# Kernel tuning notes

Measured on AMD Instinct MI355X. Metric: run time of the kernel, lower is better.

The kernel has to match this reference:

```python
import jax, jax.numpy as jnp
import numpy as np
import math

MID = 48       # mid_channels
HEADS = 4      # num_heads
POS = 16       # mid_channels // 3 (row/col positional channels)


def _unfold(x, p):
    """nn.Unfold with kernel p, padding p//2: (..., H, W) -> (..., p, p, H, W)."""
    H, W = x.shape[-2], x.shape[-1]
    pad = p // 2
    xp = jnp.pad(x, [(0, 0)] * (x.ndim - 2) + [(pad, pad), (pad, pad)])
    return jnp.stack(
        [jnp.stack([xp[..., k:k + H, l:l + W] for l in range(p)], axis=-3)
         for k in range(p)], axis=-4)


def _pe_mlp(idx, w1, b1, g, b, w2, b2):
    """Conv2d(1->16,1x1) -> LayerNorm(16) -> Swish -> Conv2d(16->POS,1x1) on scalar coords."""
    t = idx.reshape(-1, 1)                         # (N,1)
    h = t @ w1.T + b1                              # (N,16)
    mu = jnp.mean(h, -1, keepdims=True)
    var = jnp.var(h, -1, keepdims=True)
    h = (h - mu) * jax.lax.rsqrt(var + 1e-5) * g + b
    h = h * jax.nn.sigmoid(h)                      # Swish
    e = h @ w2.T + b2                              # (N,POS)
    return e.reshape(idx.shape + (e.shape[-1],))   # (V,P,P,POS)


def setup_inputs() -> dict:
    key = jax.random.key(0)
    ks = jax.random.split(key, 32)
    B, Cin, G, H, W, P, Cout = 2, 32, 4, 28, 28, 7, 64

    def n(k, shp, s=0.05):
        return jax.random.normal(k, shp, dtype=jnp.float32) * s

    inp = {"x": jax.random.normal(ks[0], (B, Cin, G, H, W), dtype=jnp.float32)}
    inp["Wq"] = n(ks[1], (MID * HEADS, Cin)); inp["bq"] = n(ks[2], (MID * HEADS,))
    inp["Wk"] = n(ks[3], (MID * HEADS, Cin)); inp["bk"] = n(ks[4], (MID * HEADS,))
    inp["Wv"] = n(ks[5], (MID * HEADS, Cin)); inp["bv"] = n(ks[6], (MID * HEADS,))
    inp["Wout"] = n(ks[7], (Cout, MID * HEADS)); inp["bout"] = n(ks[8], (Cout,))
    inp["row_w1"] = n(ks[9], (16, 1)); inp["row_b1"] = n(ks[10], (16,))
    inp["row_ln_g"] = jnp.ones((16,), jnp.float32); inp["row_ln_b"] = jnp.zeros((16,), jnp.float32)
    inp["row_w2"] = n(ks[11], (POS, 16)); inp["row_b2"] = n(ks[12], (POS,))
    inp["col_w1"] = n(ks[13], (16, 1)); inp["col_b1"] = n(ks[14], (16,))
    inp["col_ln_g"] = jnp.ones((16,), jnp.float32); inp["col_ln_b"] = jnp.zeros((16,), jnp.float32)
    inp["col_w2"] = n(ks[15], (POS, 16)); inp["col_b2"] = n(ks[16], (POS,))
    inp["group_emb"] = n(ks[17], (G, MID - 2 * POS))
    # rotated relative spatial positions, normalized to [-1, 1]
    lin = np.linspace(-1.0, 1.0, P).astype(np.float32)
    r = np.repeat(lin[:, None], P, 1)
    c = np.repeat(lin[None, :], P, 0)
    rows, cols = [], []
    for v in range(G):
        th = v * math.pi / 2.0
        rows.append(math.cos(th) * r - math.sin(th) * c)
        cols.append(math.sin(th) * r + math.cos(th) * c)
    inp["row_indices"] = jnp.asarray(np.stack(rows, 0))
    inp["col_indices"] = jnp.asarray(np.stack(cols, 0))
    # acted relative group positions for cyclic group C4
    ar = np.arange(G)
    gi = (ar[:, None, None] + ar[None, None, :] - ar[None, :, None]) % G
    inp["g_indices"] = jnp.asarray(gi, dtype=jnp.int32)
    return inp


def _forward(x, Wq, bq, Wk, bk, Wv, bv, Wout, bout,
             row_w1, row_b1, row_ln_g, row_ln_b, row_w2, row_b2,
             col_w1, col_b1, col_ln_g, col_ln_b, col_w2, col_b2,
             group_emb, row_indices, col_indices, g_indices):
    B, Cin, G, H, W = x.shape
    P = row_indices.shape[-1]
    sqn = jnp.sqrt(jnp.float32(Cin))

    def proj(Wm, bm):  # 1x1 Conv3d -> (B, MID, HEADS, G, H, W)
        y = jnp.einsum('oi,bigyx->bogyx', Wm, x) + bm[None, :, None, None, None]
        return y.reshape(B, MID, HEADS, G, H, W)

    q = proj(Wq, bq)
    k = proj(Wk, bk)
    v = proj(Wv, bv)
    k_loc = _unfold(k, P)   # (B, MID, HEADS, G, P, P, H, W)
    v_loc = _unfold(v, P)

    content = jnp.einsum('bchgij,bchmklij->bhgijmkl', q, k_loc)
    row_e = _pe_mlp(row_indices, row_w1, row_b1, row_ln_g, row_ln_b, row_w2, row_b2)
    col_e = _pe_mlp(col_indices, col_w1, col_b1, col_ln_g, col_ln_b, col_w2, col_b2)
    row_s = jnp.einsum('bchgij,vklc->bhvgijkl', q[:, :POS], row_e)
    col_s = jnp.einsum('bchgij,vklc->bhvgijkl', q[:, POS:2 * POS], col_e)
    g_e = group_emb[g_indices]                              # (V, G, M, gdim)
    g_s = jnp.einsum('bchgij,vgmc->bhvgijm', q[:, 2 * POS:], g_e)

    # scores: (b, h, v, g, i, j, m, k, l)
    scores = (row_s[:, :, :, :, :, :, None] + col_s[:, :, :, :, :, :, None]
              + g_s[..., None, None] + content[:, :, None]) / sqn

    # mask patch positions that fall outside the image (-inf -> prob 0)
    valid = _unfold(jnp.ones((H, W), jnp.float32), P)       # (P, P, H, W)
    valid = jnp.transpose(valid, (2, 3, 0, 1))[None, None, None, None, :, :, None, :, :]
    scores = jnp.where(valid > 0.5, scores, -jnp.inf)

    shp = scores.shape
    probs = jax.nn.softmax(scores.reshape(shp[:-3] + (-1,)), axis=-1).reshape(shp)

    o = jnp.einsum('bhvgijmkl,bchmklij->bchvij', probs, v_loc)  # (B, MID, HEADS, V, H, W)
    o = o.reshape(B, MID * HEADS, G, H, W)
    return jnp.einsum('oi,bivyx->bovyx', Wout, o) + bout[None, :, None, None, None]


def reference(x, Wq, bq, Wk, bk, Wv, bv, Wout, bout,
              row_w1, row_b1, row_ln_g, row_ln_b, row_w2, row_b2,
              col_w1, col_b1, col_ln_g, col_ln_b, col_w2, col_b2,
              group_emb, row_indices, col_indices, g_indices):
    return _forward(x, Wq, bq, Wk, bk, Wv, bv, Wout, bout,
                    row_w1, row_b1, row_ln_g, row_ln_b, row_w2, row_b2,
                    col_w1, col_b1, col_ln_g, col_ln_b, col_w2, col_b2,
                    group_emb, row_indices, col_indices, g_indices)
```

## Files before the change

### kernel.cpp

```cpp
#include <hip/hip_runtime.h>
#include <math.h>

#define Bb   2
#define CIN  32
#define Gg   4
#define NH   4
#define Hh   28
#define Ww   28
#define HW   784
#define Pp   7
#define PP   49
#define MID  48
#define COUT 64
#define OC   192

#define QF    0
#define KF    602112
#define VF    1204224
#define OOFF  1806336
#define KBH   75264
#define KM    18816
#define VBH   75264
#define VPL   37632

#define KSCALE 0.2550611135387359f

__device__ unsigned g_peT2[Gg * PP * 16];
__device__ unsigned g_geT2[8 * 64];
__device__ float    g_WT2[OC * COUT];

typedef _Float16 h2f __attribute__((ext_vector_type(2)));

__device__ __forceinline__ unsigned packh2(float a, float b) {
    auto r = __builtin_amdgcn_cvt_pkrtz(a, b);
    return __builtin_bit_cast(unsigned, r);
}

__device__ __forceinline__ float fdot2(unsigned a, unsigned b, float c) {
    return __builtin_amdgcn_fdot2(__builtin_bit_cast(h2f, a),
                                  __builtin_bit_cast(h2f, b), c, false);
}

__device__ __forceinline__ float exp2_fast(float x) {
    float r;
    asm("v_exp_f32 %0, %1" : "=v"(r) : "v"(x));
    return r;
}

__device__ __forceinline__ void conv7x2(const float4* __restrict__ Wr4, float bias,
                                        const float* __restrict__ x0,
                                        const float* __restrict__ x1,
                                        float* a0, float* a1) {
    float4 w[8];
    #pragma unroll
    for (int t = 0; t < 8; t++) w[t] = Wr4[t];
    #pragma unroll
    for (int jj = 0; jj < 7; jj++) { a0[jj] = bias; a1[jj] = bias; }
    #pragma unroll
    for (int ci8 = 0; ci8 < 8; ci8++) {
        int cb = ci8 * 4;
#define CH1(WV, CI, XR, A)                                                    \
        {   float wv = WV;                                                    \
            float4 xA = *(const float4*)&XR[(CI) * 8];                        \
            float4 xB = *(const float4*)&XR[(CI) * 8 + 4];                    \
            A[0] += wv * xA.x; A[1] += wv * xA.y; A[2] += wv * xA.z;          \
            A[3] += wv * xA.w; A[4] += wv * xB.x; A[5] += wv * xB.y;          \
            A[6] += wv * xB.z; }
        CH1(w[ci8].x, cb + 0, x0, a0) CH1(w[ci8].x, cb + 0, x1, a1)
        CH1(w[ci8].y, cb + 1, x0, a0) CH1(w[ci8].y, cb + 1, x1, a1)
        CH1(w[ci8].z, cb + 2, x0, a0) CH1(w[ci8].z, cb + 2, x1, a1)
        CH1(w[ci8].w, cb + 3, x0, a0) CH1(w[ci8].w, cb + 3, x1, a1)
#undef CH1
    }
}

__global__ __launch_bounds__(192) void qkvpe_kernel(const float* __restrict__ x,
    const float* __restrict__ Wq, const float* __restrict__ bq,
    const float* __restrict__ Wk, const float* __restrict__ bk,
    const float* __restrict__ Wv, const float* __restrict__ bv,
    const float* row_w1, const float* row_b1,
    const float* row_g,  const float* row_bb,
    const float* row_w2, const float* row_b2,
    const float* col_w1, const float* col_b1,
    const float* col_g,  const float* col_bb,
    const float* col_w2, const float* col_b2,
    const float* row_idx, const float* col_idx,
    const float* group_emb, const int* g_indices,
    const float* Wout,
    float* __restrict__ ws)
{
    __shared__ float xs[2 * CIN * 8];
    __shared__ float wtmp[16 * 193];
    int tid = threadIdx.x;
    unsigned* uw = (unsigned*)ws;
    if (blockIdx.x == Bb * 2 * Hh * 4) {
        for (int t = tid; t < 2 * Gg * PP; t += 192) {
            int half = t / (Gg * PP);
            int n    = t - half * (Gg * PP);
            int v = n / PP, kl = n % PP;
            const float* w1 = half ? col_w1 : row_w1;
            const float* b1 = half ? col_b1 : row_b1;
            const float* lg = half ? col_g  : row_g;
            const float* lb = half ? col_bb : row_bb;
            const float* w2 = half ? col_w2 : row_w2;
            const float* b2 = half ? col_b2 : row_b2;
            float tv = half ? col_idx[n] : row_idx[n];

            float hb[16];
            float mean = 0.f;
            for (int k = 0; k < 16; k++) { hb[k] = tv * w1[k] + b1[k]; mean += hb[k]; }
            mean *= (1.f / 16.f);
            float var = 0.f;
            for (int k = 0; k < 16; k++) { float d = hb[k] - mean; var += d * d; }
            var *= (1.f / 16.f);
            float inv = 1.f / sqrtf(var + 1e-5f);
            for (int k = 0; k < 16; k++) {
                float hn = (hb[k] - mean) * inv * lg[k] + lb[k];
                hb[k] = hn / (1.f + expf(-hn));
            }
            float accv[16];
            for (int p = 0; p < 16; p++) {
                float acc = b2[p];
                for (int k = 0; k < 16; k++) acc += hb[k] * w2[p * 16 + k];
                accv[p] = acc * KSCALE;
            }
            for (int i2 = 0; i2 < 8; i2++)
                g_peT2[(v * PP + kl) * 16 + half * 8 + i2] =
                    packh2(accv[2 * i2], accv[2 * i2 + 1]);
        }
        for (int t = tid; t < 64; t += 192) {
            int gi = g_indices[t];
            for (int i2 = 0; i2 < 8; i2++)
                g_geT2[i2 * 64 + t] = packh2(group_emb[gi * 16 + 2 * i2] * KSCALE,
                                             group_emb[gi * 16 + 2 * i2 + 1] * KSCALE);
        }
        for (int chunk = 0; chunk < 4; chunk++) {
            int obase = chunk * 16;
            __syncthreads();
            for (int idx = tid; idx < 16 * OC; idx += 192) {
                int ol = idx / OC, t = idx % OC;
                wtmp[ol * 193 + t] = Wout[(obase + ol) * OC + t];
            }
            __syncthreads();
            for (int idx = tid; idx < 16 * OC; idx += 192) {
                int tp = idx / 16, ol = idx % 16;
                int h = tp / MID, c = tp % MID;
                g_WT2[tp * 64 + obase + ol] = wtmp[ol * 193 + c * NH + h];
            }
        }
        return;
    }

    int r = blockIdx.x;
    int jq = r & 3; r >>= 2;
    int i = r % Hh; r /= Hh;
    int gp = r & 1; int b = r >> 1;
    int j0 = jq * 7;

    for (int idx = tid; idx < 2 * CIN * 7; idx += 192) {
        int gs = idx / (CIN * 7), rem = idx % (CIN * 7);
        int ci = rem / 7, jj = rem % 7;
        xs[gs * CIN * 8 + ci * 8 + jj] =
            x[((b * CIN + ci) * Gg + 2 * gp + gs) * HW + i * Ww + j0 + jj];
    }
    __syncthreads();

    int h = tid / MID, c = tid % MID;
    int oo = c * NH + h;
    int bh = b * NH + h;
    int ij0 = i * Ww + j0;
    const float* xs0 = &xs[0];
    const float* xs1 = &xs[CIN * 8];

    float a0[7], a1[7];
    conv7x2((const float4*)(Wq + oo * CIN), bq[oo], xs0, xs1, a0, a1);
    {
        int ob0 = QF + ((bh * Gg + 2 * gp + 0) * HW + ij0) * 24 + (c >> 1);
        int ob1 = QF + ((bh * Gg + 2 * gp + 1) * HW + ij0) * 24 + (c >> 1);
        #pragma unroll
        for (int jj = 0; jj < 7; jj++) {
            float p0 = __shfl_xor(a0[jj], 1, 64);
            float p1 = __shfl_xor(a1[jj], 1, 64);
            if (!(tid & 1)) {
                uw[ob0 + jj * 24] = packh2(a0[jj], p0);
                uw[ob1 + jj * 24] = packh2(a1[jj], p1);
            }
        }
    }
    conv7x2((const float4*)(Wk + oo * CIN), bk[oo], xs0, xs1, a0, a1);
    {
        int ob0 = KF + ((bh * Gg + 2 * gp + 0) * HW + ij0) * 24 + (c >> 1);
        int ob1 = KF + ((bh * Gg + 2 * gp + 1) * HW + ij0) * 24 + (c >> 1);
        #pragma unroll
        for (int jj = 0; jj < 7; jj++) {
            float v0 = a0[jj] * KSCALE, v1 = a1[jj] * KSCALE;
            float p0 = __shfl_xor(v0, 1, 64);
            float p1 = __shfl_xor(v1, 1, 64);
            if (!(tid & 1)) {
                uw[ob0 + jj * 24] = packh2(v0, p0);
                uw[ob1 + jj * 24] = packh2(v1, p1);
            }
        }
    }
    conv7x2((const float4*)(Wv + oo * CIN), bv[oo], xs0, xs1, a0, a1);
    {
        int vb = VF + ((bh * 2 + gp) * HW + ij0) * 48 + c;
        #pragma unroll
        for (int jj = 0; jj < 7; jj++)
            uw[vb + jj * 48] = packh2(a0[jj], a1[jj]);
    }
}

__global__ __launch_bounds__(256, 4) void attn_kernel(float* __restrict__ ws)
{
    __shared__ __align__(16) unsigned kvb[7000];
    __shared__ __align__(16) unsigned pp2[4][PP][8];
    __shared__ __align__(16) unsigned qp[4][4][32];
    __shared__ __align__(16) float gsm[4][64];

    const int tid  = threadIdx.x;
    const int wave = tid >> 6;
    const int lane = tid & 63;

    int blk = blockIdx.x;
    int j0 = (blk % 7) * 4;
    int i  = (blk / 7) % Hh;
    int bh = blk / (7 * Hh);
    int b = bh >> 2, h = bh & 3;
    int j  = j0 + wave;
    int ij = i * Ww + j;

    const unsigned* uw = (const unsigned*)ws;
    const unsigned* Kf = uw + KF + bh * KBH;
    const unsigned* Vf = uw + VF + bh * VBH;
    float* Ot = ws + OOFF;

    if (lane < 48) {
        int g = lane / 12, c4 = lane % 12;
        uint2 qv = *(const uint2*)&uw[QF + ((bh * Gg + g) * HW + ij) * 24 + c4 * 2];
        qp[wave][g][c4 * 2]     = qv.x;
        qp[wave][g][c4 * 2 + 1] = qv.y;
    }

    #pragma unroll
    for (int s = 0; s < 2; s++) {
        int t = tid + s * 256;
        if (t < 420) {
            int c8 = t % 6, cl = t / 6;
            int gy = i - 3 + cl / 10, gx = j0 - 3 + cl % 10;
            gy = min(max(gy, 0), Hh - 1); gx = min(max(gx, 0), Ww - 1);
            const unsigned* kp = &Kf[(gy * Ww + gx) * 24 + c8 * 4];
            #pragma unroll
            for (int m = 0; m < 4; m++) {
                uint4 kv = *(const uint4*)(kp + m * KM);
                int o = (m * 70 + cl) * 25 + c8 * 4;
                *(uint2*)&kvb[o]     = make_uint2(kv.x, kv.y);
                *(uint2*)&kvb[o + 2] = make_uint2(kv.z, kv.w);
            }
        }
    }

    int kk = lane / Pp, ll = lane % Pp;
    int cell = (lane < PP) ? kk * 10 + ll + wave : 0;
    bool vmask = (lane < PP) && ((unsigned)(i + kk - 3) < Hh) && ((unsigned)(j + ll - 3) < Ww);
    int lclamp = lane < PP ? lane : 0;

    float per[4][4] = {};
    #pragma unroll
    for (int u4 = 0; u4 < 4; u4++) {
        uint4 qA = *(const uint4*)&qp[wave][0][u4 * 4];
        uint4 qB = *(const uint4*)&qp[wave][1][u4 * 4];
        uint4 qC = *(const uint4*)&qp[wave][2][u4 * 4];
        uint4 qD = *(const uint4*)&qp[wave][3][u4 * 4];
        #pragma unroll
        for (int v = 0; v < 4; v++) {
            uint4 pk = *(const uint4*)&g_peT2[(v * PP + lclamp) * 16 + u4 * 4];
            per[v][0] = fdot2(pk.w, qA.w, fdot2(pk.z, qA.z, fdot2(pk.y, qA.y, fdot2(pk.x, qA.x, per[v][0]))));
            per[v][1] = fdot2(pk.w, qB.w, fdot2(pk.z, qB.z, fdot2(pk.y, qB.y, fdot2(pk.x, qB.x, per[v][1]))));
            per[v][2] = fdot2(pk.w, qC.w, fdot2(pk.z, qC.z, fdot2(pk.y, qC.y, fdot2(pk.x, qC.x, per[v][2]))));
            per[v][3] = fdot2(pk.w, qD.w, fdot2(pk.z, qD.z, fdot2(pk.y, qD.y, fdot2(pk.x, qD.x, per[v][3]))));
        }
    }
    if (!vmask) {
        #pragma unroll
        for (int v = 0; v < 4; v++)
            #pragma unroll
            for (int g = 0; g < 4; g++) per[v][g] = -INFINITY;
    }

    {
        int g = (lane >> 2) & 3;
        float ga = 0.f;
        #pragma unroll
        for (int u = 0; u < 8; u++)
            ga = fdot2(g_geT2[u * 64 + lane], qp[wave][g][16 + u], ga);
        gsm[wave][lane] = ga;
    }
    __syncthreads();

    float acc[4][4] = {};
    #pragma unroll 2
    for (int u4 = 0; u4 < 6; u4++) {
        uint4 qA = *(const uint4*)&qp[wave][0][u4 * 4];
        uint4 qB = *(const uint4*)&qp[wave][1][u4 * 4];
        uint4 qC = *(const uint4*)&qp[wave][2][u4 * 4];
        uint4 qD = *(const uint4*)&qp[wave][3][u4 * 4];
        #pragma unroll
        for (int m = 0; m < 4; m++) {
            int base = (m * 70 + cell) * 25 + u4 * 4;
            uint2 k01 = *(const uint2*)&kvb[base];
            uint2 k23 = *(const uint2*)&kvb[base + 2];
            acc[m][0] = fdot2(k23.y, qA.w, fdot2(k23.x, qA.z, fdot2(k01.y, qA.y, fdot2(k01.x, qA.x, acc[m][0]))));
            acc[m][1] = fdot2(k23.y, qB.w, fdot2(k23.x, qB.z, fdot2(k01.y, qB.y, fdot2(k01.x, qB.x, acc[m][1]))));
            acc[m][2] = fdot2(k23.y, qC.w, fdot2(k23.x, qC.z, fdot2(k01.y, qC.y, fdot2(k01.x, qC.x, acc[m][2]))));
            acc[m][3] = fdot2(k23.y, qD.w, fdot2(k23.x, qD.z, fdot2(k01.y, qD.y, fdot2(k01.x, qD.x, acc[m][3]))));
        }
    }

    float ppr[4][4] = {};
    #pragma unroll
    for (int v = 0; v < 4; v++) {
        #pragma unroll
        for (int g = 0; g < 4; g++) {
            int vg = v * 4 + g;
            float4 gs = *(const float4*)&gsm[wave][vg * 4];
            float ex[4];
            ex[0] = exp2_fast(acc[0][g] + per[v][g] + gs.x);
            ex[1] = exp2_fast(acc[1][g] + per[v][g] + gs.y);
            ex[2] = exp2_fast(acc[2][g] + per[v][g] + gs.z);
            ex[3] = exp2_fast(acc[3][g] + per[v][g] + gs.w);
            float ls = ex[0] + ex[1] + ex[2] + ex[3];
            #pragma unroll
            for (int d = 32; d > 0; d >>= 1) ls += __shfl_xor(ls, d, 64);
            float rinv = 1.0f / ls;
            #pragma unroll
            for (int m = 0; m < 4; m++) ppr[v][m] += ex[m] * rinv;
        }
    }
    if (lane < PP) {
        uint4 w0, w1;
        w0.x = packh2(ppr[0][0], ppr[0][1]); w0.y = packh2(ppr[0][2], ppr[0][3]);
        w0.z = packh2(ppr[1][0], ppr[1][1]); w0.w = packh2(ppr[1][2], ppr[1][3]);
        w1.x = packh2(ppr[2][0], ppr[2][1]); w1.y = packh2(ppr[2][2], ppr[2][3]);
        w1.z = packh2(ppr[3][0], ppr[3][1]); w1.w = packh2(ppr[3][2], ppr[3][3]);
        *(uint4*)&pp2[wave][lane][0] = w0;
        *(uint4*)&pp2[wave][lane][4] = w1;
    }
    __syncthreads();

    for (int t = tid; t < 840; t += 256) {
        int c4 = t % 12, cl = t / 12;
        int gy = i - 3 + cl / 10, gx = j0 - 3 + cl % 10;
        gy = min(max(gy, 0), Hh - 1); gx = min(max(gx, 0), Ww - 1);
        int off = (gy * Ww + gx) * 48 + c4 * 4;
        uint4 A = *(const uint4*)&Vf[off];
        uint4 B = *(const uint4*)&Vf[VPL + off];
        int o = cl * 48 + c4 * 4;
        *(uint4*)&kvb[o]        = A;
        *(uint4*)&kvb[3360 + o] = B;
    }
    __syncthreads();

    if (lane < MID) {
        float o0 = 0.f, o1 = 0.f, o2 = 0.f, o3 = 0.f;
        const uint4* ppw = (const uint4*)&pp2[wave][0][0];
        const unsigned* v0b = &kvb[wave * 48 + lane];
        const unsigned* v1b = v0b + 3360;
        #pragma unroll
        for (int kl2 = 0; kl2 < PP; kl2++) {
            int cellc = (kl2 / Pp) * 10 + (kl2 % Pp);
            unsigned vv0 = v0b[cellc * 48];
            unsigned vv1 = v1b[cellc * 48];
            uint4 A = ppw[kl2 * 2];
            uint4 B = ppw[kl2 * 2 + 1];
            o0 = fdot2(vv1, A.y, fdot2(vv0, A.x, o0));
            o1 = fdot2(vv1, A.w, fdot2(vv0, A.z, o1));
            o2 = fdot2(vv1, B.y, fdot2(vv0, B.x, o2));
            o3 = fdot2(vv1, B.w, fdot2(vv0, B.z, o3));
        }
        Ot[((size_t)(b * Gg + 0) * HW + ij) * OC + h * MID + lane] = o0;
        Ot[((size_t)(b * Gg + 1) * HW + ij) * OC + h * MID + lane] = o1;
        Ot[((size_t)(b * Gg + 2) * HW + ij) * OC + h * MID + lane] = o2;
        Ot[((size_t)(b * Gg + 3) * HW + ij) * OC + h * MID + lane] = o3;
    }
}

__global__ __launch_bounds__(256) void outproj_kernel(const float* __restrict__ bout,
                                                      const float* __restrict__ ws,
                                                      float* __restrict__ out)
{
    __shared__ float ov[16 * 193];
    __shared__ float res[64 * 17];
    int tid = threadIdx.x;
    int p0 = blockIdx.x * 16;
    const float* Ot = ws + OOFF;

    for (int idx = tid; idx < 16 * OC; idx += 256) {
        int pl = idx / OC, t = idx % OC;
        ov[pl * 193 + t] = Ot[(size_t)(p0 + pl) * OC + t];
    }
    __syncthreads();

    int o = tid & 63, pg = tid >> 6;
    float a0 = bout[o], a1 = a0, a2 = a0, a3 = a0;
    #pragma unroll 8
    for (int t = 0; t < OC; t++) {
        float w = g_WT2[t * 64 + o];
        a0 += w * ov[(pg     ) * 193 + t];
        a1 += w * ov[(pg +  4) * 193 + t];
        a2 += w * ov[(pg +  8) * 193 + t];
        a3 += w * ov[(pg + 12) * 193 + t];
    }
    res[o * 17 + pg     ] = a0;
    res[o * 17 + pg +  4] = a1;
    res[o * 17 + pg +  8] = a2;
    res[o * 17 + pg + 12] = a3;
    __syncthreads();

    for (int idx = tid; idx < 1024; idx += 256) {
        int o2 = idx >> 4, pl = idx & 15;
        int p = p0 + pl;
        int ij2 = p % HW; int bv = p / HW; int v = bv & 3; int bb = bv >> 2;
        out[((bb * COUT + o2) * Gg + v) * HW + ij2] = res[o2 * 17 + pl];
    }
}

extern "C" void kernel_launch(void* const* d_in, const int* in_sizes, int n_in,
                              void* d_out, int out_size, void* d_ws, size_t ws_size,
                              hipStream_t stream)
{
    const float* x      = (const float*)d_in[0];
    const float* Wq     = (const float*)d_in[1];
    const float* bq     = (const float*)d_in[2];
    const float* Wk     = (const float*)d_in[3];
    const float* bk     = (const float*)d_in[4];
    const float* Wv     = (const float*)d_in[5];
    const float* bv     = (const float*)d_in[6];
    const float* Wout   = (const float*)d_in[7];
    const float* bout   = (const float*)d_in[8];
    const float* row_w1 = (const float*)d_in[9];
    const float* row_b1 = (const float*)d_in[10];
    const float* row_g  = (const float*)d_in[11];
    const float* row_bb = (const float*)d_in[12];
    const float* row_w2 = (const float*)d_in[13];
    const float* row_b2 = (const float*)d_in[14];
    const float* col_w1 = (const float*)d_in[15];
    const float* col_b1 = (const float*)d_in[16];
    const float* col_g  = (const float*)d_in[17];
    const float* col_bb = (const float*)d_in[18];
    const float* col_w2 = (const float*)d_in[19];
    const float* col_b2 = (const float*)d_in[20];
    const float* gemb   = (const float*)d_in[21];
    const float* ridx   = (const float*)d_in[22];
    const float* cidx   = (const float*)d_in[23];
    const int*   gidx   = (const int*)d_in[24];

    float* ws  = (float*)d_ws;
    float* out = (float*)d_out;

    qkvpe_kernel<<<Bb * 2 * Hh * 4 + 1, 192, 0, stream>>>(
        x, Wq, bq, Wk, bk, Wv, bv,
        row_w1, row_b1, row_g, row_bb, row_w2, row_b2,
        col_w1, col_b1, col_g, col_bb, col_w2, col_b2,
        ridx, cidx, gemb, gidx, Wout, ws);
    attn_kernel<<<Bb * NH * Hh * (Ww / 4), 256, 0, stream>>>(ws);
    outproj_kernel<<<Bb * Gg * HW / 16, 256, 0, stream>>>(bout, ws, out);
}
```

Baseline: 187.5 us.

## Pre-transpose QKV weights in a separate prep kernel for coalesced loads

Moves the positional-embedding, group-embedding and Wout transposition setup into a new two-block prep kernel, which also writes transposed copies of Wq, Wk and Wv. The QKV projection kernel now maps threads so consecutive threads read consecutive output channels, giving coalesced weight loads, and loops over Q, K and V with one code path. This targets strided per-thread weight row reads. The cost is an extra kernel launch and a serial dependency on the prep kernel, plus extra global scratch for the transposed weights.

Result: slower. 207.6 us (+10.7%).

```diff
diff --git a/kernel.cpp b/kernel.cpp
--- a/kernel.cpp
+++ b/kernel.cpp
@@ -28,6 +28,9 @@
 __device__ unsigned g_peT2[Gg * PP * 16];
 __device__ unsigned g_geT2[8 * 64];
 __device__ float    g_WT2[OC * COUT];
+__device__ float    g_WqT[CIN * OC];
+__device__ float    g_WkT[CIN * OC];
+__device__ float    g_WvT[CIN * OC];
 
 typedef _Float16 h2f __attribute__((ext_vector_type(2)));
 
@@ -47,37 +50,7 @@
     return r;
 }
 
-__device__ __forceinline__ void conv7x2(const float4* __restrict__ Wr4, float bias,
-                                        const float* __restrict__ x0,
-                                        const float* __restrict__ x1,
-                                        float* a0, float* a1) {
-    float4 w[8];
-    #pragma unroll
-    for (int t = 0; t < 8; t++) w[t] = Wr4[t];
-    #pragma unroll
-    for (int jj = 0; jj < 7; jj++) { a0[jj] = bias; a1[jj] = bias; }
-    #pragma unroll
-    for (int ci8 = 0; ci8 < 8; ci8++) {
-        int cb = ci8 * 4;
-#define CH1(WV, CI, XR, A)                                                    \
-        {   float wv = WV;                                                    \
-            float4 xA = *(const float4*)&XR[(CI) * 8];                        \
-            float4 xB = *(const float4*)&XR[(CI) * 8 + 4];                    \
-            A[0] += wv * xA.x; A[1] += wv * xA.y; A[2] += wv * xA.z;          \
-            A[3] += wv * xA.w; A[4] += wv * xB.x; A[5] += wv * xB.y;          \
-            A[6] += wv * xB.z; }
-        CH1(w[ci8].x, cb + 0, x0, a0) CH1(w[ci8].x, cb + 0, x1, a1)
-        CH1(w[ci8].y, cb + 1, x0, a0) CH1(w[ci8].y, cb + 1, x1, a1)
-        CH1(w[ci8].z, cb + 2, x0, a0) CH1(w[ci8].z, cb + 2, x1, a1)
-        CH1(w[ci8].w, cb + 3, x0, a0) CH1(w[ci8].w, cb + 3, x1, a1)
-#undef CH1
-    }
-}
-
-__global__ __launch_bounds__(192) void qkvpe_kernel(const float* __restrict__ x,
-    const float* __restrict__ Wq, const float* __restrict__ bq,
-    const float* __restrict__ Wk, const float* __restrict__ bk,
-    const float* __restrict__ Wv, const float* __restrict__ bv,
+__global__ __launch_bounds__(256) void prep_kernel(
     const float* row_w1, const float* row_b1,
     const float* row_g,  const float* row_bb,
     const float* row_w2, const float* row_b2,
@@ -87,69 +60,84 @@
     const float* row_idx, const float* col_idx,
     const float* group_emb, const int* g_indices,
     const float* Wout,
-    float* __restrict__ ws)
+    const float* __restrict__ Wq, const float* __restrict__ Wk,
+    const float* __restrict__ Wv)
+{
+    __shared__ float wtmp[16 * 193];
+    int tid = threadIdx.x;
+    if (blockIdx.x == 1) {
+        for (int idx = tid; idx < OC * CIN; idx += 256) {
+            int oo = idx >> 5, ci = idx & 31;
+            int tp = ci * OC + oo;
+            g_WqT[tp] = Wq[idx];
+            g_WkT[tp] = Wk[idx];
+            g_WvT[tp] = Wv[idx];
+        }
+        return;
+    }
+    for (int t = tid; t < 2 * Gg * PP; t += 256) {
+        int half = t / (Gg * PP);
+        int n    = t - half * (Gg * PP);
+        int v = n / PP, kl = n % PP;
+        const float* w1 = half ? col_w1 : row_w1;
+        const float* b1 = half ? col_b1 : row_b1;
+        const float* lg = half ? col_g  : row_g;
+        const float* lb = half ? col_bb : row_bb;
+        const float* w2 = half ? col_w2 : row_w2;
+        const float* b2 = half ? col_b2 : row_b2;
+        float tv = half ? col_idx[n] : row_idx[n];
+
+        float hb[16];
+        float mean = 0.f;
+        for (int k = 0; k < 16; k++) { hb[k] = tv * w1[k] + b1[k]; mean += hb[k]; }
+        mean *= (1.f / 16.f);
+        float var = 0.f;
+        for (int k = 0; k < 16; k++) { float d = hb[k] - mean; var += d * d; }
+        var *= (1.f / 16.f);
+        float inv = 1.f / sqrtf(var + 1e-5f);
+        for (int k = 0; k < 16; k++) {
+            float hn = (hb[k] - mean) * inv * lg[k] + lb[k];
+            hb[k] = hn / (1.f + expf(-hn));
+        }
+        float accv[16];
+        for (int p = 0; p < 16; p++) {
+            float acc = b2[p];
+            for (int k = 0; k < 16; k++) acc += hb[k] * w2[p * 16 + k];
+            accv[p] = acc * KSCALE;
+        }
+        for (int i2 = 0; i2 < 8; i2++)
+            g_peT2[(v * PP + kl) * 16 + half * 8 + i2] =
+                packh2(accv[2 * i2], accv[2 * i2 + 1]);
+    }
+    for (int t = tid; t < 64; t += 256) {
+        int gi = g_indices[t];
+        for (int i2 = 0; i2 < 8; i2++)
+            g_geT2[i2 * 64 + t] = packh2(group_emb[gi * 16 + 2 * i2] * KSCALE,
+                                         group_emb[gi * 16 + 2 * i2 + 1] * KSCALE);
+    }
+    for (int chunk = 0; chunk < 4; chunk++) {
+        int obase = chunk * 16;
+        __syncthreads();
+        for (int idx = tid; idx < 16 * OC; idx += 256) {
+            int ol = idx / OC, t = idx % OC;
+            wtmp[ol * 193 + t] = Wout[(obase + ol) * OC + t];
+        }
+        __syncthreads();
+        for (int idx = tid; idx < 16 * OC; idx += 256) {
+            int tp = idx / 16, ol = idx % 16;
+            int h = tp / MID, c = tp % MID;
+            g_WT2[tp * 64 + obase + ol] = wtmp[ol * 193 + c * NH + h];
+        }
+    }
+}
+
+__global__ __launch_bounds__(192) void qkvpe_kernel(const float* __restrict__ x,
+    const float* __restrict__ bq, const float* __restrict__ bk,
+    const float* __restrict__ bv, float* __restrict__ ws)
 {
     __shared__ float xs[2 * CIN * 8];
-    __shared__ float wtmp[16 * 193];
     int tid = threadIdx.x;
     unsigned* uw = (unsigned*)ws;
-    if (blockIdx.x == Bb * 2 * Hh * 4) {
-        for (int t = tid; t < 2 * Gg * PP; t += 192) {
-            int half = t / (Gg * PP);
-            int n    = t - half * (Gg * PP);
-            int v = n / PP, kl = n % PP;
-            const float* w1 = half ? col_w1 : row_w1;
-            const float* b1 = half ? col_b1 : row_b1;
-            const float* lg = half ? col_g  : row_g;
-            const float* lb = half ? col_bb : row_bb;
-            const float* w2 = half ? col_w2 : row_w2;
-            const float* b2 = half ? col_b2 : row_b2;
-            float tv = half ? col_idx[n] : row_idx[n];
-
-            float hb[16];
-            float mean = 0.f;
-            for (int k = 0; k < 16; k++) { hb[k] = tv * w1[k] + b1[k]; mean += hb[k]; }
-            mean *= (1.f / 16.f);
-            float var = 0.f;
-            for (int k = 0; k < 16; k++) { float d = hb[k] - mean; var += d * d; }
-            var *= (1.f / 16.f);
-            float inv = 1.f / sqrtf(var + 1e-5f);
-            for (int k = 0; k < 16; k++) {
-                float hn = (hb[k] - mean) * inv * lg[k] + lb[k];
-                hb[k] = hn / (1.f + expf(-hn));
-            }
-            float accv[16];
-            for (int p = 0; p < 16; p++) {
-                float acc = b2[p];
-                for (int k = 0; k < 16; k++) acc += hb[k] * w2[p * 16 + k];
-                accv[p] = acc * KSCALE;
-            }
-            for (int i2 = 0; i2 < 8; i2++)
-                g_peT2[(v * PP + kl) * 16 + half * 8 + i2] =
-                    packh2(accv[2 * i2], accv[2 * i2 + 1]);
-        }
-        for (int t = tid; t < 64; t += 192) {
-            int gi = g_indices[t];
-            for (int i2 = 0; i2 < 8; i2++)
-                g_geT2[i2 * 64 + t] = packh2(group_emb[gi * 16 + 2 * i2] * KSCALE,
-                                             group_emb[gi * 16 + 2 * i2 + 1] * KSCALE);
-        }
-        for (int chunk = 0; chunk < 4; chunk++) {
-            int obase = chunk * 16;
-            __syncthreads();
-            for (int idx = tid; idx < 16 * OC; idx += 192) {
-                int ol = idx / OC, t = idx % OC;
-                wtmp[ol * 193 + t] = Wout[(obase + ol) * OC + t];
-            }
-            __syncthreads();
-            for (int idx = tid; idx < 16 * OC; idx += 192) {
-                int tp = idx / 16, ol = idx % 16;
-                int h = tp / MID, c = tp % MID;
-                g_WT2[tp * 64 + obase + ol] = wtmp[ol * 193 + c * NH + h];
-            }
-        }
-        return;
-    }
 
     int r = blockIdx.x;
     int jq = r & 3; r >>= 2;
@@ -165,49 +153,58 @@
     }
     __syncthreads();
 
-    int h = tid / MID, c = tid % MID;
-    int oo = c * NH + h;
+    int c = tid >> 2, h = tid & 3;
     int bh = b * NH + h;
     int ij0 = i * Ww + j0;
     const float* xs0 = &xs[0];
     const float* xs1 = &xs[CIN * 8];
 
-    float a0[7], a1[7];
-    conv7x2((const float4*)(Wq + oo * CIN), bq[oo], xs0, xs1, a0, a1);
-    {
-        int ob0 = QF + ((bh * Gg + 2 * gp + 0) * HW + ij0) * 24 + (c >> 1);
-        int ob1 = QF + ((bh * Gg + 2 * gp + 1) * HW + ij0) * 24 + (c >> 1);
-        #pragma unroll
-        for (int jj = 0; jj < 7; jj++) {
-            float p0 = __shfl_xor(a0[jj], 1, 64);
-            float p1 = __shfl_xor(a1[jj], 1, 64);
-            if (!(tid & 1)) {
-                uw[ob0 + jj * 24] = packh2(a0[jj], p0);
-                uw[ob1 + jj * 24] = packh2(a1[jj], p1);
+    #pragma unroll 1
+    for (int p = 0; p < 3; p++) {
+        const float* WT = (p == 0) ? g_WqT : (p == 1) ? g_WkT : g_WvT;
+        const float* bm = (p == 0) ? bq   : (p == 1) ? bk    : bv;
+        float bias = bm[tid];
+        float w[32];
+        #pragma unroll
+        for (int ci = 0; ci < 32; ci++) w[ci] = WT[ci * OC + tid];
+        float a0[7], a1[7];
+        #pragma unroll
+        for (int jj = 0; jj < 7; jj++) { a0[jj] = bias; a1[jj] = bias; }
+        #pragma unroll
+        for (int ci = 0; ci < 32; ci++) {
+            float wv = w[ci];
+            float4 xA0 = *(const float4*)&xs0[ci * 8];
+            float4 xB0 = *(const float4*)&xs0[ci * 8 + 4];
+            float4 xA1 = *(const float4*)&xs1[ci * 8];
+            float4 xB1 = *(const float4*)&xs1[ci * 8 + 4];
+            a0[0] += wv * xA0.x; a0[1] += wv * xA0.y; a0[2] += wv * xA0.z;
+            a0[3] += wv * xA0.w; a0[4] += wv * xB0.x; a0[5] += wv * xB0.y;
+            a0[6] += wv * xB0.z;
+            a1[0] += wv * xA1.x; a1[1] += wv * xA1.y; a1[2] += wv * xA1.z;
+            a1[3] += wv * xA1.w; a1[4] += wv * xB1.x; a1[5] += wv * xB1.y;
+            a1[6] += wv * xB1.z;
+        }
+        if (p < 2) {
+            float scl = p ? KSCALE : 1.0f;
+            int base0 = p ? KF : QF;
+            int ob0 = base0 + ((bh * Gg + 2 * gp + 0) * HW + ij0) * 24 + (c >> 1);
+            int ob1 = base0 + ((bh * Gg + 2 * gp + 1) * HW + ij0) * 24 + (c >> 1);
+            #pragma unroll
+            for (int jj = 0; jj < 7; jj++) {
+                float v0 = a0[jj] * scl, v1 = a1[jj] * scl;
+                float p0 = __shfl_xor(v0, 4, 64);
+                float p1 = __shfl_xor(v1, 4, 64);
+                if (!((tid >> 2) & 1)) {
+                    uw[ob0 + jj * 24] = packh2(v0, p0);
+                    uw[ob1 + jj * 24] = packh2(v1, p1);
+                }
             }
-        }
-    }
-    conv7x2((const float4*)(Wk + oo * CIN), bk[oo], xs0, xs1, a0, a1);
-    {
-        int ob0 = KF + ((bh * Gg + 2 * gp + 0) * HW + ij0) * 24 + (c >> 1);
-        int ob1 = KF + ((bh * Gg + 2 * gp + 1) * HW + ij0) * 24 + (c >> 1);
-        #pragma unroll
-        for (int jj = 0; jj < 7; jj++) {
-            float v0 = a0[jj] * KSCALE, v1 = a1[jj] * KSCALE;
-            float p0 = __shfl_xor(v0, 1, 64);
-            float p1 = __shfl_xor(v1, 1, 64);
-            if (!(tid & 1)) {
-                uw[ob0 + jj * 24] = packh2(v0, p0);
-                uw[ob1 + jj * 24] = packh2(v1, p1);
-            }
-        }
-    }
-    conv7x2((const float4*)(Wv + oo * CIN), bv[oo], xs0, xs1, a0, a1);
-    {
-        int vb = VF + ((bh * 2 + gp) * HW + ij0) * 48 + c;
-        #pragma unroll
-        for (int jj = 0; jj < 7; jj++)
-            uw[vb + jj * 48] = packh2(a0[jj], a1[jj]);
+        } else {
+            int vb = VF + ((bh * 2 + gp) * HW + ij0) * 48 + c;
+            #pragma unroll
+            for (int jj = 0; jj < 7; jj++)
+                uw[vb + jj * 48] = packh2(a0[jj], a1[jj]);
+        }
     }
 }
 
@@ -458,11 +455,11 @@
     float* ws  = (float*)d_ws;
     float* out = (float*)d_out;
 
-    qkvpe_kernel<<<Bb * 2 * Hh * 4 + 1, 192, 0, stream>>>(
-        x, Wq, bq, Wk, bk, Wv, bv,
+    prep_kernel<<<2, 256, 0, stream>>>(
         row_w1, row_b1, row_g, row_bb, row_w2, row_b2,
         col_w1, col_b1, col_g, col_bb, col_w2, col_b2,
-        ridx, cidx, gemb, gidx, Wout, ws);
+        ridx, cidx, gemb, gidx, Wout, Wq, Wk, Wv);
+    qkvpe_kernel<<<Bb * 2 * Hh * 4, 192, 0, stream>>>(x, bq, bk, bv, ws);
     attn_kernel<<<Bb * NH * Hh * (Ww / 4), 256, 0, stream>>>(ws);
     outproj_kernel<<<Bb * Gg * HW / 16, 256, 0, stream>>>(bout, ws, out);
 }
```
